# Kernel optimization log

Measured on AMD Instinct MI355X. Metric: run time of the kernel, lower is better.

The kernel has to match this reference:

```python
import jax, jax.numpy as jnp
import numpy as np

N, T, F, E, ED, H, B, C = 100000, 10, 64, 1600000, 8, 128, 2048, 2
BN_EPS = 1e-5


def setup_inputs() -> dict:
    key = jax.random.key(0)
    ks = jax.random.split(key, 16)
    inp = {
        "x": jax.random.normal(ks[0], (N, T * F), dtype=jnp.float32),
        "edge_index": jax.random.randint(ks[1], (2, E), 0, N, dtype=jnp.int64),
        "edge_attr": jax.random.normal(ks[2], (E, ED), dtype=jnp.float32),
        "ptr": jnp.sort(jax.random.randint(ks[3], (B + 1,), 0, N, dtype=jnp.int64)),
        # EdgeWeightedSAGE params
        "w_msg": jax.random.normal(ks[4], (F + ED, H), dtype=jnp.float32) * 0.05,
        "b_msg": jnp.zeros((H,), dtype=jnp.float32),
        "w_self": jax.random.normal(ks[5], (F, H), dtype=jnp.float32) * 0.05,
        "b_self": jnp.zeros((H,), dtype=jnp.float32),
        "bn_gamma": jnp.ones((H,), dtype=jnp.float32),
        "bn_beta": jnp.zeros((H,), dtype=jnp.float32),
        # LSTM params (PyTorch gate order i,f,g,o)
        "w_ih": jax.random.normal(ks[6], (4 * H, H), dtype=jnp.float32) * 0.05,
        "w_hh": jax.random.normal(ks[7], (4 * H, H), dtype=jnp.float32) * 0.05,
        "b_ih": jnp.zeros((4 * H,), dtype=jnp.float32),
        "b_hh": jnp.zeros((4 * H,), dtype=jnp.float32),
        # classifier
        "w_cls": jax.random.normal(ks[8], (H, C), dtype=jnp.float32) * 0.05,
        "b_cls": jnp.zeros((C,), dtype=jnp.float32),
    }
    return inp


def _htgnn_forward(x, edge_attr, w_msg, b_msg, w_self, b_self, bn_gamma, bn_beta,
                   w_ih, w_hh, b_ih, b_hh, w_cls, b_cls, edge_index, ptr):
    src, dst = edge_index[0], edge_index[1]
    focal_idx = ptr[:-1]  # [B]
    xs = x.reshape(N, T, F).transpose(1, 0, 2)  # [T, N, F]

    ones_e = jnp.ones((E, 1), dtype=x.dtype)
    cnt = jax.ops.segment_sum(ones_e, dst, num_segments=N)  # [N,1]
    cnt = jnp.maximum(cnt, 1.0)

    def sage_step(_, x_t):  # x_t: [N, F]
        msg_in = jnp.concatenate([x_t[src], edge_attr], axis=-1)  # [E, F+ED]
        msg = msg_in @ w_msg + b_msg                               # [E, H]
        agg = jax.ops.segment_sum(msg, dst, num_segments=N) / cnt # scatter-mean
        out = x_t @ w_self + b_self + agg                          # [N, H]
        # BatchNorm1d (training-mode batch stats, biased variance)
        mean = out.mean(axis=0)
        var = out.var(axis=0)
        out = (out - mean) * jax.lax.rsqrt(var + BN_EPS) * bn_gamma + bn_beta
        h_t = jax.nn.relu(out)
        return None, h_t[focal_idx]  # [B, H]

    _, h_seq = jax.lax.scan(sage_step, None, xs)  # [T, B, H]

    def lstm_step(carry, h_in):  # h_in: [B, H]
        h, c = carry
        gates = h_in @ w_ih.T + h @ w_hh.T + b_ih + b_hh  # [B, 4H]
        i, f, g, o = jnp.split(gates, 4, axis=-1)
        i, f, o = jax.nn.sigmoid(i), jax.nn.sigmoid(f), jax.nn.sigmoid(o)
        g = jnp.tanh(g)
        c = f * c + i * g
        h = o * jnp.tanh(c)
        return (h, c), None

    h0 = jnp.zeros((h_seq.shape[1], H), dtype=x.dtype)
    (h_n, _), _ = jax.lax.scan(lstm_step, (h0, h0), h_seq)

    return h_n @ w_cls + b_cls  # [B, C]


def reference(x, edge_index, edge_attr, ptr, w_msg, b_msg, w_self, b_self,
              bn_gamma, bn_beta, w_ih, w_hh, b_ih, b_hh, w_cls, b_cls):
    return _htgnn_forward(x, edge_attr, w_msg, b_msg, w_self, b_self,
                          bn_gamma, bn_beta, w_ih, w_hh, b_ih, b_hh,
                          w_cls, b_cls, edge_index, ptr)
```

## Files before the change

kernel.cpp:

```cpp
#include <hip/hip_runtime.h>
#include <hip/hip_bf16.h>

#define N_NODES 100000
#define T_STEPS 10
#define F_DIM   64
#define E_EDGES 1600000
#define ED_DIM  8
#define H_DIM   128
#define B_BATCH 2048
#define C_CLS   2
#define TF      640
#define K_IN    136
#define G4H     512
#define XROW    168
#define PBLK    98
#define LPITCH  136

typedef __attribute__((ext_vector_type(8))) short short8;
typedef __attribute__((ext_vector_type(4))) float f32x4;

__device__ __forceinline__ unsigned short fbs(float f) {
    __hip_bfloat16 h = __float2bfloat16(f);
    return *(unsigned short*)&h;
}
__device__ __forceinline__ float bs2f(unsigned short u) {
    unsigned int v = ((unsigned int)u) << 16;
    return __uint_as_float(v);
}
__device__ __forceinline__ unsigned int pack2(float lo, float hi) {
    return (unsigned int)fbs(lo) | ((unsigned int)fbs(hi) << 16);
}
__device__ __forceinline__ float fsig(float x) {
    return 1.0f / (1.0f + __expf(-x));
}
__device__ __forceinline__ float ftanh(float x) {
    float e = __expf(2.0f * x);
    return 1.0f - 2.0f / (e + 1.0f);
}

#define WS_DEG      0
#define WS_ROWPTR   100096
#define WS_CURSOR   200192
#define WS_INV      300288
#define WS_AGGE     400384
#define WS_SUMS     1200384
#define WS_ZEND     1202944
#define WS_CSRSRC   1202944
#define WS_AGGXB    2802944
#define WS_AGGEB    6002944
#define WS_HSEQB    6402944
#define WS_HN       7713664
#define WS_WB       7975808
#define WS_WL       7986048
#define WS_PART     8051584
#define WS_BOFF     8051712
#define WS_XB       8051840

__global__ __launch_bounds__(256) void k_xcast(const float* __restrict__ x,
                                               unsigned short* __restrict__ xb) {
    int i = blockIdx.x * blockDim.x + threadIdx.x;
    const float4* x4 = (const float4*)x;
    float4 a = x4[2 * i], b = x4[2 * i + 1];
    uint4 o;
    o.x = pack2(a.x, a.y);
    o.y = pack2(a.z, a.w);
    o.z = pack2(b.x, b.y);
    o.w = pack2(b.z, b.w);
    ((uint4*)xb)[i] = o;
}

__global__ void k_deg(const int* __restrict__ ei, int* __restrict__ deg) {
    int e = blockIdx.x * blockDim.x + threadIdx.x;
    if (e < E_EDGES) atomicAdd(&deg[ei[E_EDGES + e]], 1);
}

__global__ __launch_bounds__(1024) void k_part(const int* __restrict__ deg,
                                               int* __restrict__ part) {
    __shared__ int red[1024];
    int gid = blockIdx.x * 1024 + threadIdx.x;
    red[threadIdx.x] = (gid < N_NODES) ? deg[gid] : 0;
    __syncthreads();
    for (int off = 512; off > 0; off >>= 1) {
        if (threadIdx.x < off) red[threadIdx.x] += red[threadIdx.x + off];
        __syncthreads();
    }
    if (threadIdx.x == 0) part[blockIdx.x] = red[0];
}

__global__ __launch_bounds__(128) void k_scanpart(const int* __restrict__ part,
        int* __restrict__ boff, int* __restrict__ rowptr) {
    __shared__ int buf[128];
    int li = threadIdx.x;
    int v = (li < PBLK) ? part[li] : 0;
    buf[li] = v;
    __syncthreads();
    for (int off = 1; off < 128; off <<= 1) {
        int u = (li >= off) ? buf[li - off] : 0;
        __syncthreads();
        buf[li] += u;
        __syncthreads();
    }
    if (li < PBLK) boff[li] = buf[li] - v;
    if (li == 0) rowptr[N_NODES] = E_EDGES;
}

__global__ __launch_bounds__(1024) void k_rowfill(const int* __restrict__ deg,
        const int* __restrict__ boff, int* __restrict__ rowptr,
        int* __restrict__ cursor, float* __restrict__ inv) {
    __shared__ int buf[1024];
    int li = threadIdx.x;
    int gid = blockIdx.x * 1024 + li;
    int d = (gid < N_NODES) ? deg[gid] : 0;
    buf[li] = d;
    __syncthreads();
    for (int off = 1; off < 1024; off <<= 1) {
        int u = (li >= off) ? buf[li - off] : 0;
        __syncthreads();
        buf[li] += u;
        __syncthreads();
    }
    if (gid < N_NODES) {
        int excl = boff[blockIdx.x] + buf[li] - d;
        rowptr[gid] = excl;
        cursor[gid] = excl;
        inv[gid] = 1.0f / (float)(d > 1 ? d : 1);
    }
}

__global__ void k_fill(const int* __restrict__ ei, int* __restrict__ cursor,
                       int* __restrict__ csr_src) {
    int e = blockIdx.x * blockDim.x + threadIdx.x;
    if (e < E_EDGES) {
        int dst = ei[E_EDGES + e];
        int pos = atomicAdd(&cursor[dst], 1);
        csr_src[pos] = ei[e];
    }
}

__global__ void k_agge(const int* __restrict__ ei, const float* __restrict__ ea,
                       float* __restrict__ agge) {
    int i = blockIdx.x * blockDim.x + threadIdx.x;
    if (i < E_EDGES * ED_DIM) {
        int e = i >> 3, j = i & 7;
        int dst = ei[E_EDGES + e];
        atomicAdd(&agge[dst * ED_DIM + j], ea[i]);
    }
}

__global__ void k_scale_agge(float* __restrict__ agge, const float* __restrict__ inv,
                             unsigned short* __restrict__ aggeb) {
    int i = blockIdx.x * blockDim.x + threadIdx.x;
    if (i < N_NODES * ED_DIM) {
        float v = agge[i] * inv[i >> 3];
        agge[i] = v;
        aggeb[i] = fbs(v);
    }
}

__global__ void k_wprep(const float* __restrict__ wself, const float* __restrict__ wmsg,
                        unsigned short* __restrict__ wB) {
    int i = blockIdx.x * blockDim.x + threadIdx.x;
    if (i < 20480) {
        int j = i & 7, q = (i >> 3) & 3, n = (i >> 5) & 127, kt = i >> 12;
        int k = kt * 32 + q * 8 + j;
        float v = 0.f;
        if (k < 64)       v = wself[k * 128 + n];
        else if (k < 136) v = wmsg[(k - 64) * 128 + n];
        wB[i] = fbs(v);
    }
}

__global__ void k_wlstm(const float* __restrict__ wih, const float* __restrict__ whh,
                        unsigned short* __restrict__ wL) {
    int i = blockIdx.x * blockDim.x + threadIdx.x;
    if (i < 131072) {
        int j8 = i & 7, q = (i >> 3) & 3, np = (i >> 5) & 511, kt = i >> 14;
        int k = kt * 32 + q * 8 + j8;
        int hsub = np >> 6, gate = (np >> 4) & 3, hlo = np & 15;
        int j = gate * 128 + hsub * 16 + hlo;
        float v = (k < 128) ? wih[j * H_DIM + k] : whh[j * H_DIM + (k - 128)];
        wL[i] = fbs(v);
    }
}

__global__ __launch_bounds__(256) void k_gather(const unsigned short* __restrict__ xb,
        const int* __restrict__ rowptr, const int* __restrict__ csr_src,
        const float* __restrict__ inv, unsigned short* __restrict__ aggxb, int t) {
    int node = blockIdx.x * 4 + (threadIdx.x >> 6);
    int lane = threadIdx.x & 63;
    int half = lane >> 5, li = lane & 31;
    int beg = rowptr[node], end = rowptr[node + 1];
    const unsigned short* xt = xb + t * F_DIM + 2 * li;
    float a0 = 0.f, a1 = 0.f;
    int e = beg;
    for (; e + 7 < end; e += 8) {
        int s0 = csr_src[e + half];
        int s1 = csr_src[e + 2 + half];
        int s2 = csr_src[e + 4 + half];
        int s3 = csr_src[e + 6 + half];
        unsigned int u0 = *(const unsigned int*)&xt[(size_t)s0 * TF];
        unsigned int u1 = *(const unsigned int*)&xt[(size_t)s1 * TF];
        unsigned int u2 = *(const unsigned int*)&xt[(size_t)s2 * TF];
        unsigned int u3 = *(const unsigned int*)&xt[(size_t)s3 * TF];
        a0 += __uint_as_float(u0 << 16) + __uint_as_float(u1 << 16)
            + __uint_as_float(u2 << 16) + __uint_as_float(u3 << 16);
        a1 += __uint_as_float(u0 & 0xffff0000u) + __uint_as_float(u1 & 0xffff0000u)
            + __uint_as_float(u2 & 0xffff0000u) + __uint_as_float(u3 & 0xffff0000u);
    }
    if (e + 3 < end) {
        int s0 = csr_src[e + half], s1 = csr_src[e + 2 + half];
        unsigned int u0 = *(const unsigned int*)&xt[(size_t)s0 * TF];
        unsigned int u1 = *(const unsigned int*)&xt[(size_t)s1 * TF];
        a0 += __uint_as_float(u0 << 16) + __uint_as_float(u1 << 16);
        a1 += __uint_as_float(u0 & 0xffff0000u) + __uint_as_float(u1 & 0xffff0000u);
        e += 4;
    }
    if (e + 1 < end) {
        int s = csr_src[e + half];
        unsigned int u = *(const unsigned int*)&xt[(size_t)s * TF];
        a0 += __uint_as_float(u << 16);
        a1 += __uint_as_float(u & 0xffff0000u);
        e += 2;
    }
    if (half == 0 && e < end) {
        int s = csr_src[e];
        unsigned int u = *(const unsigned int*)&xt[(size_t)s * TF];
        a0 += __uint_as_float(u << 16);
        a1 += __uint_as_float(u & 0xffff0000u);
    }
    a0 += __shfl_xor(a0, 32, 64);
    a1 += __shfl_xor(a1, 32, 64);
    if (lane < 32) {
        float iv = inv[node];
        *(unsigned int*)&aggxb[node * F_DIM + 2 * li] = pack2(a0 * iv, a1 * iv);
    }
}

__global__ __launch_bounds__(256) void k_stats(const unsigned short* __restrict__ xb,
        const unsigned short* __restrict__ aggxb, const unsigned short* __restrict__ aggeb,
        const unsigned short* __restrict__ wB, float* __restrict__ sums, int t) {
    __shared__ __align__(16) unsigned short s_xa[32 * XROW];
    int tid  = threadIdx.x;
    int wave = tid >> 6, lane = tid & 63;
    int q = lane >> 4, m = lane & 15;
    int n0 = wave * 32;

    short8 bf[5][2];
    #pragma unroll
    for (int kt = 0; kt < 5; kt++) {
        bf[kt][0] = *(const short8*)&wB[kt * 4096 + (n0 + m) * 32 + q * 8];
        bf[kt][1] = *(const short8*)&wB[kt * 4096 + (n0 + 16 + m) * 32 + q * 8];
    }

    float cs0 = 0.f, cq0 = 0.f, cs1 = 0.f, cq1 = 0.f;

    for (int tile = blockIdx.x; tile < N_NODES / 32; tile += gridDim.x) {
        int row0 = tile * 32;
        __syncthreads();
        for (int i = tid; i < 32 * 20; i += 256) {
            int r = i / 20, qq = i - r * 20;
            int n = row0 + r;
            uint4 v = make_uint4(0, 0, 0, 0);
            if (qq < 8)        v = *(const uint4*)&xb[(size_t)n * TF + t * F_DIM + qq * 8];
            else if (qq < 16)  v = *(const uint4*)&aggxb[n * F_DIM + (qq - 8) * 8];
            else if (qq == 16) v = *(const uint4*)&aggeb[n * ED_DIM];
            *(uint4*)&s_xa[r * XROW + qq * 8] = v;
        }
        __syncthreads();

        f32x4 a00 = {0.f,0.f,0.f,0.f}, a01 = a00, a10 = a00, a11 = a00;
        #pragma unroll
        for (int kt = 0; kt < 5; kt++) {
            short8 af0 = *(const short8*)&s_xa[m * XROW + kt * 32 + q * 8];
            short8 af1 = *(const short8*)&s_xa[(16 + m) * XROW + kt * 32 + q * 8];
            a00 = __builtin_amdgcn_mfma_f32_16x16x32_bf16(af0, bf[kt][0], a00, 0, 0, 0);
            a10 = __builtin_amdgcn_mfma_f32_16x16x32_bf16(af1, bf[kt][0], a10, 0, 0, 0);
            a01 = __builtin_amdgcn_mfma_f32_16x16x32_bf16(af0, bf[kt][1], a01, 0, 0, 0);
            a11 = __builtin_amdgcn_mfma_f32_16x16x32_bf16(af1, bf[kt][1], a11, 0, 0, 0);
        }
        #pragma unroll
        for (int g = 0; g < 4; g++) {
            float v0 = a00[g], v1 = a10[g];
            cs0 += v0 + v1;
            cq0 += v0 * v0 + v1 * v1;
            float w0 = a01[g], w1 = a11[g];
            cs1 += w0 + w1;
            cq1 += w0 * w0 + w1 * w1;
        }
    }

    cs0 += __shfl_xor(cs0, 16, 64); cq0 += __shfl_xor(cq0, 16, 64);
    cs0 += __shfl_xor(cs0, 32, 64); cq0 += __shfl_xor(cq0, 32, 64);
    cs1 += __shfl_xor(cs1, 16, 64); cq1 += __shfl_xor(cq1, 16, 64);
    cs1 += __shfl_xor(cs1, 32, 64); cq1 += __shfl_xor(cq1, 32, 64);
    if (lane < 16) {
        atomicAdd(&sums[n0 + m], cs0);
        atomicAdd(&sums[128 + n0 + m], cq0);
        atomicAdd(&sums[n0 + 16 + m], cs1);
        atomicAdd(&sums[128 + n0 + 16 + m], cq1);
    }
}

__global__ __launch_bounds__(128) void k_focal(const float* __restrict__ x,
        const unsigned short* __restrict__ aggxb, const float* __restrict__ agge,
        const float* __restrict__ wself, const float* __restrict__ wmsg,
        const float* __restrict__ sums, const float* __restrict__ gamma,
        const float* __restrict__ beta, const int* __restrict__ ptr,
        unsigned short* __restrict__ hseqb, int t) {
    __shared__ float s_xin[K_IN];
    int b   = blockIdx.x;
    int n   = ptr[b];
    int tid = threadIdx.x;
    if (tid < K_IN - 64) {
        int k = 64 + tid;
        s_xin[k] = (k < 128) ? bs2f(aggxb[n * F_DIM + (k - 64)])
                             : agge[n * ED_DIM + (k - 128)];
    }
    {
        int k = tid & 63;
        s_xin[k] = x[(size_t)n * TF + t * F_DIM + k];
    }
    __syncthreads();
    int h = tid;
    float acc = 0.f;
    #pragma unroll 8
    for (int k = 0; k < F_DIM; k++) acc += s_xin[k] * wself[k * H_DIM + h];
    #pragma unroll 8
    for (int k = 0; k < 72; k++)    acc += s_xin[F_DIM + k] * wmsg[k * H_DIM + h];
    float mean = sums[h] * (1.0f / N_NODES);
    float var  = sums[H_DIM + h] * (1.0f / N_NODES) - mean * mean;
    var = fmaxf(var, 0.f);
    float istd = 1.0f / sqrtf(var + 1e-5f);
    float sc = gamma[h] * istd;
    float sh = beta[h] - mean * sc;
    float v = fmaxf(acc * sc + sh, 0.f);
    hseqb[(size_t)(t * B_BATCH + b) * H_DIM + h] = fbs(v);
}

__global__ __launch_bounds__(512) void k_lstm_all(const unsigned short* __restrict__ hseqb,
        const unsigned short* __restrict__ wL, const float* __restrict__ bih,
        const float* __restrict__ bhh, float* __restrict__ hn) {
    __shared__ __align__(16) unsigned short s_hin[16 * LPITCH];
    __shared__ __align__(16) unsigned short s_h[16 * LPITCH];
    int tid = threadIdx.x, w = tid >> 6, lane = tid & 63;
    int q = lane >> 4, hlo = lane & 15;
    int row0 = blockIdx.x * 16;
    for (int i = tid; i < 16 * LPITCH / 8; i += 512)
        ((uint4*)s_h)[i] = make_uint4(0, 0, 0, 0);
    float c[4] = {0.f, 0.f, 0.f, 0.f};
    float bias[4];
    #pragma unroll
    for (int nt = 0; nt < 4; nt++) {
        int j = nt * 128 + w * 16 + hlo;
        bias[nt] = bih[j] + bhh[j];
    }
    short8 bfr[8][4];
    #pragma unroll
    for (int kt = 0; kt < 8; kt++)
        #pragma unroll
        for (int nt = 0; nt < 4; nt++)
            bfr[kt][nt] = *(const short8*)&wL[((kt * 512) + (w * 64 + nt * 16 + hlo)) * 32 + q * 8];

    for (int t = 0; t < T_STEPS; t++) {
        if (tid < 256) {
            int r = tid >> 4, cc = tid & 15;
            ((uint4*)&s_hin[r * LPITCH])[cc] =
                ((const uint4*)(hseqb + (size_t)(t * B_BATCH + row0 + r) * H_DIM))[cc];
        }
        __syncthreads();
        f32x4 acc[4];
        #pragma unroll
        for (int nt = 0; nt < 4; nt++) acc[nt] = (f32x4){0.f, 0.f, 0.f, 0.f};
        #pragma unroll
        for (int kt = 0; kt < 8; kt++) {
            const unsigned short* abase = (kt < 4) ? s_hin : s_h;
            int ko = (kt & 3) * 32 + q * 8;
            short8 am = *(const short8*)&abase[hlo * LPITCH + ko];
            #pragma unroll
            for (int nt = 0; nt < 4; nt++)
                acc[nt] = __builtin_amdgcn_mfma_f32_16x16x32_bf16(am, bfr[kt][nt], acc[nt], 0, 0, 0);
        }
        __syncthreads();
        #pragma unroll
        for (int r = 0; r < 4; r++) {
            float gi = acc[0][r] + bias[0];
            float gf = acc[1][r] + bias[1];
            float gg = acc[2][r] + bias[2];
            float go = acc[3][r] + bias[3];
            float si = fsig(gi);
            float sf = fsig(gf);
            float so = fsig(go);
            float tg = ftanh(gg);
            float cn = sf * c[r] + si * tg;
            c[r] = cn;
            float hv = so * ftanh(cn);
            int row = q * 4 + r;
            s_h[row * LPITCH + w * 16 + hlo] = fbs(hv);
            if (t == T_STEPS - 1)
                hn[(size_t)(row0 + row) * H_DIM + w * 16 + hlo] = hv;
        }
    }
}

__global__ void k_cls(const float* __restrict__ h, const float* __restrict__ wcls,
                      const float* __restrict__ bcls, float* __restrict__ out) {
    int i = blockIdx.x * blockDim.x + threadIdx.x;
    if (i < B_BATCH * C_CLS) {
        int b = i >> 1, cc = i & 1;
        float acc = bcls[cc];
        for (int k = 0; k < H_DIM; k++) acc += h[b * H_DIM + k] * wcls[k * C_CLS + cc];
        out[i] = acc;
    }
}

extern "C" void kernel_launch(void* const* d_in, const int* in_sizes, int n_in,
                              void* d_out, int out_size, void* d_ws, size_t ws_size,
                              hipStream_t stream) {
    const float* x     = (const float*)d_in[0];
    const int*   ei    = (const int*)d_in[1];
    const float* ea    = (const float*)d_in[2];
    const int*   ptr   = (const int*)d_in[3];
    const float* wmsg  = (const float*)d_in[4];
    const float* wself = (const float*)d_in[6];
    const float* gamma = (const float*)d_in[8];
    const float* beta  = (const float*)d_in[9];
    const float* wih   = (const float*)d_in[10];
    const float* whh   = (const float*)d_in[11];
    const float* bih   = (const float*)d_in[12];
    const float* bhh   = (const float*)d_in[13];
    const float* wcls  = (const float*)d_in[14];
    const float* bcls  = (const float*)d_in[15];
    float* out = (float*)d_out;

    float* ws = (float*)d_ws;
    int*            deg    = (int*)(ws + WS_DEG);
    int*            rowptr = (int*)(ws + WS_ROWPTR);
    int*            cursor = (int*)(ws + WS_CURSOR);
    float*          inv    = ws + WS_INV;
    float*          agge   = ws + WS_AGGE;
    float*          sums   = ws + WS_SUMS;
    int*            csrs   = (int*)(ws + WS_CSRSRC);
    unsigned short* aggxb  = (unsigned short*)(ws + WS_AGGXB);
    unsigned short* aggeb  = (unsigned short*)(ws + WS_AGGEB);
    unsigned short* hseqb  = (unsigned short*)(ws + WS_HSEQB);
    float*          hn     = ws + WS_HN;
    unsigned short* wB     = (unsigned short*)(ws + WS_WB);
    unsigned short* wL     = (unsigned short*)(ws + WS_WL);
    int*            part   = (int*)(ws + WS_PART);
    int*            boff   = (int*)(ws + WS_BOFF);
    unsigned short* xb     = (unsigned short*)(ws + WS_XB);

    hipMemsetAsync(ws, 0, (size_t)WS_ZEND * 4, stream);

    k_xcast<<<31250, 256, 0, stream>>>(x, xb);
    k_deg<<<(E_EDGES + 255) / 256, 256, 0, stream>>>(ei, deg);
    k_part<<<PBLK, 1024, 0, stream>>>(deg, part);
    k_scanpart<<<1, 128, 0, stream>>>(part, boff, rowptr);
    k_rowfill<<<PBLK, 1024, 0, stream>>>(deg, boff, rowptr, cursor, inv);
    k_agge<<<(E_EDGES * ED_DIM + 255) / 256, 256, 0, stream>>>(ei, ea, agge);
    k_scale_agge<<<(N_NODES * ED_DIM + 255) / 256, 256, 0, stream>>>(agge, inv, aggeb);
    k_fill<<<(E_EDGES + 255) / 256, 256, 0, stream>>>(ei, cursor, csrs);
    k_wprep<<<80, 256, 0, stream>>>(wself, wmsg, wB);
    k_wlstm<<<512, 256, 0, stream>>>(wih, whh, wL);

    for (int t = 0; t < T_STEPS; t++) {
        float* sums_t = sums + t * 256;
        k_gather<<<N_NODES / 4, 256, 0, stream>>>(xb, rowptr, csrs, inv, aggxb, t);
        k_stats<<<512, 256, 0, stream>>>(xb, aggxb, aggeb, wB, sums_t, t);
        k_focal<<<B_BATCH, 128, 0, stream>>>(x, aggxb, agge, wself, wmsg, sums_t,
                                             gamma, beta, ptr, hseqb, t);
    }
    k_lstm_all<<<B_BATCH / 16, 512, 0, stream>>>(hseqb, wL, bih, bhh, hn);
    k_cls<<<(B_BATCH * C_CLS + 255) / 256, 256, 0, stream>>>(hn, wcls, bcls, out);
}
```

Measured before the change: 1.579 ms.

## Batch all time steps into single gather, stats and focal kernels

Replaces the per-time-step loop of gather, stats and focal launches with one launch of each kernel that handles all ten time steps. The gather now reads the full 640-wide bf16 row of each source node once per edge, instead of one 64-wide slice per step, so CSR indices are read once and row reads are contiguous. Stats and focal loop over time internally with per-step accumulators. This trades 30 launches and repeated index traffic for a larger aggregated buffer, placed at a new workspace offset, and more registers per thread.

```diff
diff --git a/kernel.cpp b/kernel.cpp
--- a/kernel.cpp
+++ b/kernel.cpp
@@ -46,7 +46,6 @@
 #define WS_SUMS     1200384
 #define WS_ZEND     1202944
 #define WS_CSRSRC   1202944
-#define WS_AGGXB    2802944
 #define WS_AGGEB    6002944
 #define WS_HSEQB    6402944
 #define WS_HN       7713664
@@ -55,6 +54,7 @@
 #define WS_PART     8051584
 #define WS_BOFF     8051712
 #define WS_XB       8051840
+#define WS_AGGXB    40051840
 
 __global__ __launch_bounds__(256) void k_xcast(const float* __restrict__ x,
                                                unsigned short* __restrict__ xb) {
@@ -183,62 +183,51 @@
     }
 }
 
-__global__ __launch_bounds__(256) void k_gather(const unsigned short* __restrict__ xb,
+__global__ __launch_bounds__(256) void k_gather_all(const unsigned short* __restrict__ xb,
         const int* __restrict__ rowptr, const int* __restrict__ csr_src,
-        const float* __restrict__ inv, unsigned short* __restrict__ aggxb, int t) {
+        const float* __restrict__ inv, unsigned short* __restrict__ aggxb) {
     int node = blockIdx.x * 4 + (threadIdx.x >> 6);
     int lane = threadIdx.x & 63;
-    int half = lane >> 5, li = lane & 31;
     int beg = rowptr[node], end = rowptr[node + 1];
-    const unsigned short* xt = xb + t * F_DIM + 2 * li;
-    float a0 = 0.f, a1 = 0.f;
+    float a[10];
+    #pragma unroll
+    for (int c = 0; c < 10; c++) a[c] = 0.f;
+    const unsigned int* xbu = (const unsigned int*)xb;
     int e = beg;
-    for (; e + 7 < end; e += 8) {
-        int s0 = csr_src[e + half];
-        int s1 = csr_src[e + 2 + half];
-        int s2 = csr_src[e + 4 + half];
-        int s3 = csr_src[e + 6 + half];
-        unsigned int u0 = *(const unsigned int*)&xt[(size_t)s0 * TF];
-        unsigned int u1 = *(const unsigned int*)&xt[(size_t)s1 * TF];
-        unsigned int u2 = *(const unsigned int*)&xt[(size_t)s2 * TF];
-        unsigned int u3 = *(const unsigned int*)&xt[(size_t)s3 * TF];
-        a0 += __uint_as_float(u0 << 16) + __uint_as_float(u1 << 16)
-            + __uint_as_float(u2 << 16) + __uint_as_float(u3 << 16);
-        a1 += __uint_as_float(u0 & 0xffff0000u) + __uint_as_float(u1 & 0xffff0000u)
-            + __uint_as_float(u2 & 0xffff0000u) + __uint_as_float(u3 & 0xffff0000u);
-    }
-    if (e + 3 < end) {
-        int s0 = csr_src[e + half], s1 = csr_src[e + 2 + half];
-        unsigned int u0 = *(const unsigned int*)&xt[(size_t)s0 * TF];
-        unsigned int u1 = *(const unsigned int*)&xt[(size_t)s1 * TF];
-        a0 += __uint_as_float(u0 << 16) + __uint_as_float(u1 << 16);
-        a1 += __uint_as_float(u0 & 0xffff0000u) + __uint_as_float(u1 & 0xffff0000u);
-        e += 4;
-    }
-    if (e + 1 < end) {
-        int s = csr_src[e + half];
-        unsigned int u = *(const unsigned int*)&xt[(size_t)s * TF];
-        a0 += __uint_as_float(u << 16);
-        a1 += __uint_as_float(u & 0xffff0000u);
-        e += 2;
-    }
-    if (half == 0 && e < end) {
-        int s = csr_src[e];
-        unsigned int u = *(const unsigned int*)&xt[(size_t)s * TF];
-        a0 += __uint_as_float(u << 16);
-        a1 += __uint_as_float(u & 0xffff0000u);
-    }
-    a0 += __shfl_xor(a0, 32, 64);
-    a1 += __shfl_xor(a1, 32, 64);
-    if (lane < 32) {
-        float iv = inv[node];
-        *(unsigned int*)&aggxb[node * F_DIM + 2 * li] = pack2(a0 * iv, a1 * iv);
-    }
-}
-
-__global__ __launch_bounds__(256) void k_stats(const unsigned short* __restrict__ xb,
+    for (; e + 1 < end; e += 2) {
+        int s0 = csr_src[e], s1 = csr_src[e + 1];
+        const unsigned int* r0 = xbu + (size_t)s0 * 320 + lane;
+        const unsigned int* r1 = xbu + (size_t)s1 * 320 + lane;
+        unsigned int u0[5], u1[5];
+        #pragma unroll
+        for (int c = 0; c < 5; c++) { u0[c] = r0[c * 64]; u1[c] = r1[c * 64]; }
+        #pragma unroll
+        for (int c = 0; c < 5; c++) {
+            a[2 * c]     += __uint_as_float(u0[c] << 16) + __uint_as_float(u1[c] << 16);
+            a[2 * c + 1] += __uint_as_float(u0[c] & 0xffff0000u)
+                          + __uint_as_float(u1[c] & 0xffff0000u);
+        }
+    }
+    if (e < end) {
+        int s0 = csr_src[e];
+        const unsigned int* r0 = xbu + (size_t)s0 * 320 + lane;
+        #pragma unroll
+        for (int c = 0; c < 5; c++) {
+            unsigned int u = r0[c * 64];
+            a[2 * c]     += __uint_as_float(u << 16);
+            a[2 * c + 1] += __uint_as_float(u & 0xffff0000u);
+        }
+    }
+    float iv = inv[node];
+    unsigned int* orow = (unsigned int*)aggxb + (size_t)node * 320 + lane;
+    #pragma unroll
+    for (int c = 0; c < 5; c++)
+        orow[c * 64] = pack2(a[2 * c] * iv, a[2 * c + 1] * iv);
+}
+
+__global__ __launch_bounds__(256) void k_stats_all(const unsigned short* __restrict__ xb,
         const unsigned short* __restrict__ aggxb, const unsigned short* __restrict__ aggeb,
-        const unsigned short* __restrict__ wB, float* __restrict__ sums, int t) {
+        const unsigned short* __restrict__ wB, float* __restrict__ sums) {
     __shared__ __align__(16) unsigned short s_xa[32 * XROW];
     int tid  = threadIdx.x;
     int wave = tid >> 6, lane = tid & 63;
@@ -252,89 +241,107 @@
         bf[kt][1] = *(const short8*)&wB[kt * 4096 + (n0 + 16 + m) * 32 + q * 8];
     }
 
-    float cs0 = 0.f, cq0 = 0.f, cs1 = 0.f, cq1 = 0.f;
+    float cs[T_STEPS][2], cq[T_STEPS][2];
+    #pragma unroll
+    for (int t = 0; t < T_STEPS; t++) {
+        cs[t][0] = cs[t][1] = 0.f;
+        cq[t][0] = cq[t][1] = 0.f;
+    }
 
     for (int tile = blockIdx.x; tile < N_NODES / 32; tile += gridDim.x) {
         int row0 = tile * 32;
-        __syncthreads();
-        for (int i = tid; i < 32 * 20; i += 256) {
-            int r = i / 20, qq = i - r * 20;
-            int n = row0 + r;
-            uint4 v = make_uint4(0, 0, 0, 0);
-            if (qq < 8)        v = *(const uint4*)&xb[(size_t)n * TF + t * F_DIM + qq * 8];
-            else if (qq < 16)  v = *(const uint4*)&aggxb[n * F_DIM + (qq - 8) * 8];
-            else if (qq == 16) v = *(const uint4*)&aggeb[n * ED_DIM];
-            *(uint4*)&s_xa[r * XROW + qq * 8] = v;
-        }
-        __syncthreads();
-
-        f32x4 a00 = {0.f,0.f,0.f,0.f}, a01 = a00, a10 = a00, a11 = a00;
-        #pragma unroll
-        for (int kt = 0; kt < 5; kt++) {
-            short8 af0 = *(const short8*)&s_xa[m * XROW + kt * 32 + q * 8];
-            short8 af1 = *(const short8*)&s_xa[(16 + m) * XROW + kt * 32 + q * 8];
-            a00 = __builtin_amdgcn_mfma_f32_16x16x32_bf16(af0, bf[kt][0], a00, 0, 0, 0);
-            a10 = __builtin_amdgcn_mfma_f32_16x16x32_bf16(af1, bf[kt][0], a10, 0, 0, 0);
-            a01 = __builtin_amdgcn_mfma_f32_16x16x32_bf16(af0, bf[kt][1], a01, 0, 0, 0);
-            a11 = __builtin_amdgcn_mfma_f32_16x16x32_bf16(af1, bf[kt][1], a11, 0, 0, 0);
-        }
-        #pragma unroll
-        for (int g = 0; g < 4; g++) {
-            float v0 = a00[g], v1 = a10[g];
-            cs0 += v0 + v1;
-            cq0 += v0 * v0 + v1 * v1;
-            float w0 = a01[g], w1 = a11[g];
-            cs1 += w0 + w1;
-            cq1 += w0 * w0 + w1 * w1;
-        }
-    }
-
-    cs0 += __shfl_xor(cs0, 16, 64); cq0 += __shfl_xor(cq0, 16, 64);
-    cs0 += __shfl_xor(cs0, 32, 64); cq0 += __shfl_xor(cq0, 32, 64);
-    cs1 += __shfl_xor(cs1, 16, 64); cq1 += __shfl_xor(cq1, 16, 64);
-    cs1 += __shfl_xor(cs1, 32, 64); cq1 += __shfl_xor(cq1, 32, 64);
-    if (lane < 16) {
-        atomicAdd(&sums[n0 + m], cs0);
-        atomicAdd(&sums[128 + n0 + m], cq0);
-        atomicAdd(&sums[n0 + 16 + m], cs1);
-        atomicAdd(&sums[128 + n0 + 16 + m], cq1);
-    }
-}
-
-__global__ __launch_bounds__(128) void k_focal(const float* __restrict__ x,
+        #pragma unroll
+        for (int t = 0; t < T_STEPS; t++) {
+            __syncthreads();
+            for (int i = tid; i < 32 * 20; i += 256) {
+                int r = i / 20, qq = i - r * 20;
+                int n = row0 + r;
+                uint4 v = make_uint4(0, 0, 0, 0);
+                if (qq < 8)        v = *(const uint4*)&xb[(size_t)n * TF + t * F_DIM + qq * 8];
+                else if (qq < 16)  v = *(const uint4*)&aggxb[(size_t)n * TF + t * F_DIM + (qq - 8) * 8];
+                else if (qq == 16) v = *(const uint4*)&aggeb[n * ED_DIM];
+                *(uint4*)&s_xa[r * XROW + qq * 8] = v;
+            }
+            __syncthreads();
+
+            f32x4 a00 = {0.f,0.f,0.f,0.f}, a01 = a00, a10 = a00, a11 = a00;
+            #pragma unroll
+            for (int kt = 0; kt < 5; kt++) {
+                short8 af0 = *(const short8*)&s_xa[m * XROW + kt * 32 + q * 8];
+                short8 af1 = *(const short8*)&s_xa[(16 + m) * XROW + kt * 32 + q * 8];
+                a00 = __builtin_amdgcn_mfma_f32_16x16x32_bf16(af0, bf[kt][0], a00, 0, 0, 0);
+                a10 = __builtin_amdgcn_mfma_f32_16x16x32_bf16(af1, bf[kt][0], a10, 0, 0, 0);
+                a01 = __builtin_amdgcn_mfma_f32_16x16x32_bf16(af0, bf[kt][1], a01, 0, 0, 0);
+                a11 = __builtin_amdgcn_mfma_f32_16x16x32_bf16(af1, bf[kt][1], a11, 0, 0, 0);
+            }
+            #pragma unroll
+            for (int g = 0; g < 4; g++) {
+                float v0 = a00[g], v1 = a10[g];
+                cs[t][0] += v0 + v1;
+                cq[t][0] += v0 * v0 + v1 * v1;
+                float w0 = a01[g], w1 = a11[g];
+                cs[t][1] += w0 + w1;
+                cq[t][1] += w0 * w0 + w1 * w1;
+            }
+        }
+    }
+
+    #pragma unroll
+    for (int t = 0; t < T_STEPS; t++) {
+        float cs0 = cs[t][0], cq0 = cq[t][0], cs1 = cs[t][1], cq1 = cq[t][1];
+        cs0 += __shfl_xor(cs0, 16, 64); cq0 += __shfl_xor(cq0, 16, 64);
+        cs0 += __shfl_xor(cs0, 32, 64); cq0 += __shfl_xor(cq0, 32, 64);
+        cs1 += __shfl_xor(cs1, 16, 64); cq1 += __shfl_xor(cq1, 16, 64);
+        cs1 += __shfl_xor(cs1, 32, 64); cq1 += __shfl_xor(cq1, 32, 64);
+        if (lane < 16) {
+            float* st = sums + t * 256;
+            atomicAdd(&st[n0 + m], cs0);
+            atomicAdd(&st[128 + n0 + m], cq0);
+            atomicAdd(&st[n0 + 16 + m], cs1);
+            atomicAdd(&st[128 + n0 + 16 + m], cq1);
+        }
+    }
+}
+
+__global__ __launch_bounds__(128) void k_focal_all(const float* __restrict__ x,
         const unsigned short* __restrict__ aggxb, const float* __restrict__ agge,
         const float* __restrict__ wself, const float* __restrict__ wmsg,
         const float* __restrict__ sums, const float* __restrict__ gamma,
         const float* __restrict__ beta, const int* __restrict__ ptr,
-        unsigned short* __restrict__ hseqb, int t) {
+        unsigned short* __restrict__ hseqb) {
     __shared__ float s_xin[K_IN];
     int b   = blockIdx.x;
     int n   = ptr[b];
     int tid = threadIdx.x;
-    if (tid < K_IN - 64) {
-        int k = 64 + tid;
-        s_xin[k] = (k < 128) ? bs2f(aggxb[n * F_DIM + (k - 64)])
-                             : agge[n * ED_DIM + (k - 128)];
-    }
-    {
-        int k = tid & 63;
-        s_xin[k] = x[(size_t)n * TF + t * F_DIM + k];
-    }
-    __syncthreads();
     int h = tid;
-    float acc = 0.f;
-    #pragma unroll 8
-    for (int k = 0; k < F_DIM; k++) acc += s_xin[k] * wself[k * H_DIM + h];
-    #pragma unroll 8
-    for (int k = 0; k < 72; k++)    acc += s_xin[F_DIM + k] * wmsg[k * H_DIM + h];
-    float mean = sums[h] * (1.0f / N_NODES);
-    float var  = sums[H_DIM + h] * (1.0f / N_NODES) - mean * mean;
-    var = fmaxf(var, 0.f);
-    float istd = 1.0f / sqrtf(var + 1e-5f);
-    float sc = gamma[h] * istd;
-    float sh = beta[h] - mean * sc;
-    float v = fmaxf(acc * sc + sh, 0.f);
-    hseqb[(size_t)(t * B_BATCH + b) * H_DIM + h] = fbs(v);
+    float gm = gamma[h], bt = beta[h];
+    for (int t = 0; t < T_STEPS; t++) {
+        __syncthreads();
+        if (tid < K_IN - 64) {
+            int k = 64 + tid;
+            s_xin[k] = (k < 128) ? bs2f(aggxb[(size_t)n * TF + t * F_DIM + (k - 64)])
+                                 : agge[n * ED_DIM + (k - 128)];
+        }
+        {
+            int k = tid & 63;
+            s_xin[k] = x[(size_t)n * TF + t * F_DIM + k];
+        }
+        __syncthreads();
+        float acc = 0.f;
+        #pragma unroll 8
+        for (int k = 0; k < F_DIM; k++) acc += s_xin[k] * wself[k * H_DIM + h];
+        #pragma unroll 8
+        for (int k = 0; k < 72; k++)    acc += s_xin[F_DIM + k] * wmsg[k * H_DIM + h];
+        const float* st = sums + t * 256;
+        float mean = st[h] * (1.0f / N_NODES);
+        float var  = st[H_DIM + h] * (1.0f / N_NODES) - mean * mean;
+        var = fmaxf(var, 0.f);
+        float istd = 1.0f / sqrtf(var + 1e-5f);
+        float sc = gm * istd;
+        float sh = bt - mean * sc;
+        float v = fmaxf(acc * sc + sh, 0.f);
+        hseqb[(size_t)(t * B_BATCH + b) * H_DIM + h] = fbs(v);
+    }
 }
 
 __global__ __launch_bounds__(512) void k_lstm_all(const unsigned short* __restrict__ hseqb,
@@ -440,7 +447,6 @@
     float*          agge   = ws + WS_AGGE;
     float*          sums   = ws + WS_SUMS;
     int*            csrs   = (int*)(ws + WS_CSRSRC);
-    unsigned short* aggxb  = (unsigned short*)(ws + WS_AGGXB);
     unsigned short* aggeb  = (unsigned short*)(ws + WS_AGGEB);
     unsigned short* hseqb  = (unsigned short*)(ws + WS_HSEQB);
     float*          hn     = ws + WS_HN;
@@ -449,6 +455,7 @@
     int*            part   = (int*)(ws + WS_PART);
     int*            boff   = (int*)(ws + WS_BOFF);
     unsigned short* xb     = (unsigned short*)(ws + WS_XB);
+    unsigned short* aggxb  = (unsigned short*)(ws + WS_AGGXB);
 
     hipMemsetAsync(ws, 0, (size_t)WS_ZEND * 4, stream);
 
@@ -463,13 +470,10 @@
     k_wprep<<<80, 256, 0, stream>>>(wself, wmsg, wB);
     k_wlstm<<<512, 256, 0, stream>>>(wih, whh, wL);
 
-    for (int t = 0; t < T_STEPS; t++) {
-        float* sums_t = sums + t * 256;
-        k_gather<<<N_NODES / 4, 256, 0, stream>>>(xb, rowptr, csrs, inv, aggxb, t);
-        k_stats<<<512, 256, 0, stream>>>(xb, aggxb, aggeb, wB, sums_t, t);
-        k_focal<<<B_BATCH, 128, 0, stream>>>(x, aggxb, agge, wself, wmsg, sums_t,
-                                             gamma, beta, ptr, hseqb, t);
-    }
+    k_gather_all<<<N_NODES / 4, 256, 0, stream>>>(xb, rowptr, csrs, inv, aggxb);
+    k_stats_all<<<512, 256, 0, stream>>>(xb, aggxb, aggeb, wB, sums);
+    k_focal_all<<<B_BATCH, 128, 0, stream>>>(x, aggxb, agge, wself, wmsg, sums,
+                                             gamma, beta, ptr, hseqb);
     k_lstm_all<<<B_BATCH / 16, 512, 0, stream>>>(hseqb, wL, bih, bhh, hn);
     k_cls<<<(B_BATCH * C_CLS + 255) / 256, 256, 0, stream>>>(hn, wcls, bcls, out);
 }
```

After: 1.312 ms. -16.9%, faster.
